# Performance work log

Measured on AMD Instinct MI355X. Metric: run time of the kernel, lower is better.

## Reference

```python
import jax, jax.numpy as jnp
import numpy as np
import math

MAX_REL_POS = 32  # max_relative_position

def _sincos_table(d_model, max_len):
    pos = np.arange(max_len)[:, None].astype(np.float32)
    div = np.exp(np.arange(0, d_model, 2).astype(np.float32) * (-math.log(10000.0) / d_model))
    pe = np.zeros((max_len, d_model), dtype=np.float32)
    pe[:, 0::2] = np.sin(pos * div)
    pe[:, 1::2] = np.cos(pos * div)
    return jnp.asarray(pe)

def setup_inputs() -> dict:
    rng = jax.random.key(0)
    k1, k2, k3 = jax.random.split(rng, 3)
    B, H, S, D = 4, 16, 1024, 64
    pe = _sincos_table(D, 2 * MAX_REL_POS + 1)  # fixed (non-trainable) buffer
    return {
        "query": jax.random.normal(k1, (B, H, S, D), jnp.float32),
        "key": jax.random.normal(k2, (B, H, S, D), jnp.float32),
        "value": jax.random.normal(k3, (B, H, S, D), jnp.float32),
        "pe_k": pe,
        "pe_v": pe,
    }

def reference(query, key, value, pe_k, pe_v):
    B, H, S, D = query.shape
    # relative distance indices: clip(k - q, -P, P) + P  -> [S, S]
    dist = jnp.clip(jnp.arange(S)[None, :] - jnp.arange(S)[:, None],
                    -MAX_REL_POS, MAX_REL_POS) + MAX_REL_POS
    R_k = pe_k[dist]  # [S, S, D]
    R_v = pe_v[dist]  # [S, S, D]
    scores = jnp.einsum('bhqd,bhkd->bhqk', query, key)
    scores = scores + jnp.einsum('bhqd,qkd->bhqk', query, R_k)
    scores = scores / math.sqrt(D)
    # one_direction=True -> causal mask
    causal = jnp.tril(jnp.ones((S, S), dtype=bool))
    scores = jnp.where(causal[None, None], scores, jnp.float32(-1e9))
    p_attn = jax.nn.softmax(scores, axis=-1)
    output = jnp.einsum('bhqk,bhkd->bhqd', p_attn, value)
    output = output + jnp.einsum('bhqv,qvd->bhqd', p_attn, R_v)
    return output, p_attn
```

## Files before the change

### kernel.cpp

```cpp
#include <hip/hip_runtime.h>

typedef __attribute__((ext_vector_type(8))) short bfrag;
typedef __attribute__((ext_vector_type(4))) float ffrag;

namespace {
constexpr int Sc = 1024, Dc = 64;
constexpr int P2 = 72;
constexpr int PQ = 64;
constexpr int PW = 33;
constexpr float SCALE = 0.125f;
}

__device__ __forceinline__ unsigned short f2bf(float f) {
    unsigned u = __builtin_bit_cast(unsigned, f);
    u += 0x7fffu + ((u >> 16) & 1u);
    return (unsigned short)(u >> 16);
}
__device__ __forceinline__ bfrag pack8(float4 a, float4 b) {
    bfrag r;
    r[0] = (short)f2bf(a.x); r[1] = (short)f2bf(a.y);
    r[2] = (short)f2bf(a.z); r[3] = (short)f2bf(a.w);
    r[4] = (short)f2bf(b.x); r[5] = (short)f2bf(b.y);
    r[6] = (short)f2bf(b.z); r[7] = (short)f2bf(b.w);
    return r;
}
#define MFMA(a, b, c) __builtin_amdgcn_mfma_f32_16x16x32_bf16((a), (b), (c), 0, 0, 0)

__global__ __launch_bounds__(256, 2)
void relattn(const float* __restrict__ Qg, const float* __restrict__ Kg,
             const float* __restrict__ Vg, const float* __restrict__ pek,
             const float* __restrict__ pev, float* __restrict__ outg,
             float* __restrict__ pbuf)
{
    __shared__ __align__(16) char smem[72448];
    unsigned short* Ks0 = (unsigned short*)smem;
    unsigned short* Ks1 = (unsigned short*)(smem + 9216);
    unsigned short* Vt0 = (unsigned short*)(smem + 18432);
    unsigned short* Vt1 = (unsigned short*)(smem + 27648);
    unsigned short* Pt0 = (unsigned short*)(smem + 36864);
    unsigned short* Pt1 = (unsigned short*)(smem + 46080);
    float* Ts = (float*)(smem + 55296);
    unsigned short* Qs = (unsigned short*)(smem + 63744);
    float* Ws = (float*)(smem + 63744);
    float* W0 = (float*)(smem + 72192);
    float* Ot = (float*)smem;

    const int tid  = threadIdx.x;
    const int bh   = blockIdx.y;
    const int wv   = tid >> 6;
    const int lane = tid & 63;
    const int n    = lane & 15;
    const int quad = lane >> 4;

    const float* Qbh = Qg + (size_t)bh * Sc * Dc;
    const float* Kbh = Kg + (size_t)bh * Sc * Dc;
    const float* Vbh = Vg + (size_t)bh * Sc * Dc;
    float* pbh = pbuf + (size_t)bh * Sc * Sc;
    float* obh = outg + (size_t)bh * Sc * Dc;

    const int sr  = tid >> 2;
    const int sc4 = (tid & 3) * 16;
    const int kp  = tid & 31;
    const int vd0 = (tid >> 5) * 8;

    const int rr = tid >> 4;
    const int c4 = tid & 15;

    for (int half = 0; half < 2; ++half) {
        const int qt = half ? (15 - (int)blockIdx.x) : (int)blockIdx.x;
        const int qrow = wv * 16 + quad * 4;

        __syncthreads();

        float4 k0a, k0b, k0c, k0d;
        {
            const float* ksrc = Kbh + (size_t)sr * Dc + sc4;
            k0a = *(const float4*)(ksrc);
            k0b = *(const float4*)(ksrc + 4);
            k0c = *(const float4*)(ksrc + 8);
            k0d = *(const float4*)(ksrc + 12);
        }
        {
            const float* src = Qbh + (size_t)(qt * 64 + sr) * Dc + sc4;
            float4 a = *(const float4*)(src);
            float4 b = *(const float4*)(src + 4);
            float4 c = *(const float4*)(src + 8);
            float4 d = *(const float4*)(src + 12);
            *(bfrag*)&Qs[sr * PQ + sc4]     = pack8(a, b);
            *(bfrag*)&Qs[sr * PQ + sc4 + 8] = pack8(c, d);
        }
        for (int i = tid; i < 135; i += 256) {
            bfrag z = {};
            *(bfrag*)&Ks0[33 * P2 + i * 8] = z;
        }
        if (tid < 132) {
            int r = tid >> 2, c0 = (tid & 3) * 16;
            const float* src = pek + (size_t)r * Dc + c0;
            float4 a = *(const float4*)(src);
            float4 b = *(const float4*)(src + 4);
            float4 c = *(const float4*)(src + 8);
            float4 d = *(const float4*)(src + 12);
            *(bfrag*)&Ks0[r * P2 + c0]     = pack8(a, b);
            *(bfrag*)&Ks0[r * P2 + c0 + 8] = pack8(c, d);
        }
        __syncthreads();

        bfrag qa0 = *(bfrag*)&Qs[(wv * 16 + n) * PQ + quad * 8];
        bfrag qa1 = *(bfrag*)&Qs[(wv * 16 + n) * PQ + 32 + quad * 8];

        #pragma unroll
        for (int sub = 0; sub < 3; ++sub) {
            bfrag b0 = *(bfrag*)&Ks0[(sub * 16 + n) * P2 + quad * 8];
            bfrag b1 = *(bfrag*)&Ks0[(sub * 16 + n) * P2 + 32 + quad * 8];
            ffrag c = {};
            c = MFMA(qa0, b0, c);
            c = MFMA(qa1, b1, c);
            int j = sub * 16 + n;
            if (j <= 32) {
                #pragma unroll
                for (int reg = 0; reg < 4; ++reg)
                    Ts[(qrow + reg) * PW + j] = c[reg];
            }
        }
        *(bfrag*)&Ks1[sr * P2 + sc4]     = pack8(k0a, k0b);
        *(bfrag*)&Ks1[sr * P2 + sc4 + 8] = pack8(k0c, k0d);
        float4 pka, pkb, pkc, pkd;
        if (qt >= 1) {
            const float* ksrc = Kbh + (size_t)(64 + sr) * Dc + sc4;
            pka = *(const float4*)(ksrc);
            pkb = *(const float4*)(ksrc + 4);
            pkc = *(const float4*)(ksrc + 8);
            pkd = *(const float4*)(ksrc + 12);
        }
        __syncthreads();

        float ts0[4];
        #pragma unroll
        for (int reg = 0; reg < 4; ++reg) ts0[reg] = Ts[(qrow + reg) * PW];

        for (int idx = tid; idx < 64 * PW; idx += 256) Ws[idx] = 0.f;

        {
            const int zb = (qt + 1) * 64;
            if (zb < Sc) {
                const int z4 = (Sc - zb) >> 2;
                const float4 z = make_float4(0.f, 0.f, 0.f, 0.f);
                for (int r = 0; r < 64; ++r) {
                    float4* rp = (float4*)(pbh + (size_t)(qt * 64 + r) * Sc + zb);
                    for (int cz = tid; cz < z4; cz += 256) rp[cz] = z;
                }
            }
        }

        float lsum[4] = {0.f, 0.f, 0.f, 0.f};
        for (int kt = 0; kt <= qt; ++kt) {
            const bool bnd = (kt >= qt - 1);
            unsigned short* Kc = (kt & 1) ? Ks0 : Ks1;
            unsigned short* Kn = (kt & 1) ? Ks1 : Ks0;
            #pragma unroll
            for (int sub = 0; sub < 4; ++sub) {
                bfrag b0 = *(bfrag*)&Kc[(sub * 16 + n) * P2 + quad * 8];
                bfrag b1 = *(bfrag*)&Kc[(sub * 16 + n) * P2 + 32 + quad * 8];
                ffrag c = {};
                c = MFMA(qa0, b0, c);
                c = MFMA(qa1, b1, c);
                const int k = kt * 64 + sub * 16 + n;
                if (!bnd) {
                    #pragma unroll
                    for (int reg = 0; reg < 4; ++reg)
                        lsum[reg] += __expf((c[reg] + ts0[reg]) * SCALE);
                } else {
                    #pragma unroll
                    for (int reg = 0; reg < 4; ++reg) {
                        int jrel = k - (qt * 64 + qrow + reg) + 32;
                        if (jrel <= 32) {
                            int jcl = jrel < 0 ? 0 : jrel;
                            lsum[reg] += __expf((c[reg] + Ts[(qrow + reg) * PW + jcl]) * SCALE);
                        }
                    }
                }
            }
            if (kt < qt) {
                *(bfrag*)&Kn[sr * P2 + sc4]     = pack8(pka, pkb);
                *(bfrag*)&Kn[sr * P2 + sc4 + 8] = pack8(pkc, pkd);
            }
            if (kt + 2 <= qt) {
                const float* ksrc = Kbh + (size_t)((kt + 2) * 64 + sr) * Dc + sc4;
                pka = *(const float4*)(ksrc);
                pkb = *(const float4*)(ksrc + 4);
                pkc = *(const float4*)(ksrc + 8);
                pkd = *(const float4*)(ksrc + 12);
            }
            __syncthreads();
        }
        float rinv[4];
        #pragma unroll
        for (int reg = 0; reg < 4; ++reg) {
            float l = lsum[reg];
            l += __shfl_xor(l, 1);
            l += __shfl_xor(l, 2);
            l += __shfl_xor(l, 4);
            l += __shfl_xor(l, 8);
            rinv[reg] = 1.f / l;
        }

        {
            const float* ksrc = Kbh + (size_t)sr * Dc + sc4;
            float4 a = *(const float4*)(ksrc);
            float4 b = *(const float4*)(ksrc + 4);
            float4 c = *(const float4*)(ksrc + 8);
            float4 d = *(const float4*)(ksrc + 12);
            *(bfrag*)&Ks0[sr * P2 + sc4]     = pack8(a, b);
            *(bfrag*)&Ks0[sr * P2 + sc4 + 8] = pack8(c, d);
        }
        if (qt >= 1) {
            const float* ksrc = Kbh + (size_t)(64 + sr) * Dc + sc4;
            pka = *(const float4*)(ksrc);
            pkb = *(const float4*)(ksrc + 4);
            pkc = *(const float4*)(ksrc + 8);
            pkd = *(const float4*)(ksrc + 12);
        }
        float4 pva, pvb, pvc, pvd;
        {
            const float* vsrc = Vbh + (size_t)(2 * kp) * Dc + vd0;
            pva = *(const float4*)(vsrc);
            pvb = *(const float4*)(vsrc + 4);
            pvc = *(const float4*)(vsrc + Dc);
            pvd = *(const float4*)(vsrc + Dc + 4);
        }
        __syncthreads();

        ffrag oacc[4];
        #pragma unroll
        for (int i = 0; i < 4; ++i) { ffrag z = {}; oacc[i] = z; }

        for (int kt = 0; kt <= qt; ++kt) {
            const bool bnd = (kt >= qt - 1);
            unsigned short* Kc  = (kt & 1) ? Ks1 : Ks0;
            unsigned short* Kn  = (kt & 1) ? Ks0 : Ks1;
            unsigned short* Vc  = (kt & 1) ? Vt1 : Vt0;
            unsigned short* Vp  = (kt & 1) ? Vt0 : Vt1;
            unsigned short* Ptc = (kt & 1) ? Pt1 : Pt0;
            unsigned short* Ptp = (kt & 1) ? Pt0 : Pt1;

            #pragma unroll
            for (int sub = 0; sub < 4; ++sub) {
                bfrag b0 = *(bfrag*)&Kc[(sub * 16 + n) * P2 + quad * 8];
                bfrag b1 = *(bfrag*)&Kc[(sub * 16 + n) * P2 + 32 + quad * 8];
                ffrag c = {};
                c = MFMA(qa0, b0, c);
                c = MFMA(qa1, b1, c);
                const int k = kt * 64 + sub * 16 + n;
                if (!bnd) {
                    #pragma unroll
                    for (int reg = 0; reg < 4; ++reg) {
                        float p = __expf((c[reg] + ts0[reg]) * SCALE) * rinv[reg];
                        Ptc[(qrow + reg) * P2 + sub * 16 + n] = (unsigned short)f2bf(p);
                    }
                } else {
                    #pragma unroll
                    for (int reg = 0; reg < 4; ++reg) {
                        int jrel = k - (qt * 64 + qrow + reg) + 32;
                        float p = 0.f;
                        if (jrel <= 32) {
                            int jcl = jrel < 0 ? 0 : jrel;
                            p = __expf((c[reg] + Ts[(qrow + reg) * PW + jcl]) * SCALE) * rinv[reg];
                        }
                        Ptc[(qrow + reg) * P2 + sub * 16 + n] = (unsigned short)f2bf(p);
                        if ((unsigned)(jrel - 1) < 32u) Ws[(qrow + reg) * PW + jrel - 1] = p;
                    }
                }
            }
            if (kt < qt) {
                *(bfrag*)&Kn[sr * P2 + sc4]     = pack8(pka, pkb);
                *(bfrag*)&Kn[sr * P2 + sc4 + 8] = pack8(pkc, pkd);
            }
            {
                float r0[8] = {pva.x, pva.y, pva.z, pva.w, pvb.x, pvb.y, pvb.z, pvb.w};
                float r1[8] = {pvc.x, pvc.y, pvc.z, pvc.w, pvd.x, pvd.y, pvd.z, pvd.w};
                #pragma unroll
                for (int i = 0; i < 8; ++i) {
                    unsigned pk = (unsigned)f2bf(r0[i]) | ((unsigned)f2bf(r1[i]) << 16);
                    *(unsigned*)&Vc[(vd0 + i) * P2 + 2 * kp] = pk;
                }
            }
            if (kt + 2 <= qt) {
                const float* ksrc = Kbh + (size_t)((kt + 2) * 64 + sr) * Dc + sc4;
                pka = *(const float4*)(ksrc);
                pkb = *(const float4*)(ksrc + 4);
                pkc = *(const float4*)(ksrc + 8);
                pkd = *(const float4*)(ksrc + 12);
            }
            if (kt + 1 <= qt) {
                const float* vsrc = Vbh + (size_t)((kt + 1) * 64 + 2 * kp) * Dc + vd0;
                pva = *(const float4*)(vsrc);
                pvb = *(const float4*)(vsrc + 4);
                pvc = *(const float4*)(vsrc + Dc);
                pvd = *(const float4*)(vsrc + Dc + 4);
            }
            if (kt >= 1) {
                bfrag pb0 = *(bfrag*)&Ptp[(wv * 16 + n) * P2 + quad * 8];
                bfrag pb1 = *(bfrag*)&Ptp[(wv * 16 + n) * P2 + 32 + quad * 8];
                #pragma unroll
                for (int ds = 0; ds < 4; ++ds) {
                    bfrag va0 = *(bfrag*)&Vp[(ds * 16 + n) * P2 + quad * 8];
                    bfrag va1 = *(bfrag*)&Vp[(ds * 16 + n) * P2 + 32 + quad * 8];
                    oacc[ds] = MFMA(va0, pb0, oacc[ds]);
                    oacc[ds] = MFMA(va1, pb1, oacc[ds]);
                }
                float* base = pbh + ((size_t)(qt * 64 + rr) * Sc + (kt - 1) * 64 + c4 * 4);
                #pragma unroll
                for (int step = 0; step < 4; ++step) {
                    const int r = step * 16 + rr;
                    const unsigned short* ps = &Ptp[r * P2 + c4 * 4];
                    unsigned two0 = *(const unsigned*)(ps);
                    unsigned two1 = *(const unsigned*)(ps + 2);
                    float4 v;
                    v.x = __builtin_bit_cast(float, (two0 & 0xffffu) << 16);
                    v.y = __builtin_bit_cast(float, two0 & 0xffff0000u);
                    v.z = __builtin_bit_cast(float, (two1 & 0xffffu) << 16);
                    v.w = __builtin_bit_cast(float, two1 & 0xffff0000u);
                    *(float4*)(base + (size_t)(step * 16) * Sc) = v;
                }
            }
            __syncthreads();
        }
        {
            unsigned short* Ptp = (qt & 1) ? Pt1 : Pt0;
            unsigned short* Vp  = (qt & 1) ? Vt1 : Vt0;
            bfrag pb0 = *(bfrag*)&Ptp[(wv * 16 + n) * P2 + quad * 8];
            bfrag pb1 = *(bfrag*)&Ptp[(wv * 16 + n) * P2 + 32 + quad * 8];
            #pragma unroll
            for (int ds = 0; ds < 4; ++ds) {
                bfrag va0 = *(bfrag*)&Vp[(ds * 16 + n) * P2 + quad * 8];
                bfrag va1 = *(bfrag*)&Vp[(ds * 16 + n) * P2 + 32 + quad * 8];
                oacc[ds] = MFMA(va0, pb0, oacc[ds]);
                oacc[ds] = MFMA(va1, pb1, oacc[ds]);
            }
            float* base = pbh + ((size_t)(qt * 64 + rr) * Sc + qt * 64 + c4 * 4);
            #pragma unroll
            for (int step = 0; step < 4; ++step) {
                const int r = step * 16 + rr;
                const unsigned short* ps = &Ptp[r * P2 + c4 * 4];
                unsigned two0 = *(const unsigned*)(ps);
                unsigned two1 = *(const unsigned*)(ps + 2);
                float4 v;
                v.x = __builtin_bit_cast(float, (two0 & 0xffffu) << 16);
                v.y = __builtin_bit_cast(float, two0 & 0xffff0000u);
                v.z = __builtin_bit_cast(float, (two1 & 0xffffu) << 16);
                v.w = __builtin_bit_cast(float, two1 & 0xffff0000u);
                *(float4*)(base + (size_t)(step * 16) * Sc) = v;
            }
        }
        __syncthreads();

        if (tid < 64) {
            float s = 0.f;
            #pragma unroll
            for (int j = 0; j < 32; ++j) s += Ws[tid * PW + j];
            W0[tid] = 1.f - s;
        }
        {
            int q = tid >> 2, j0 = (tid & 3) * 8;
            #pragma unroll
            for (int i = 0; i < 8; i += 2) {
                unsigned pk = (unsigned)f2bf(Ws[q * PW + j0 + i]) |
                              ((unsigned)f2bf(Ws[q * PW + j0 + i + 1]) << 16);
                *(unsigned*)&Pt0[q * P2 + j0 + i] = pk;
            }
        }
        {
            int jj = tid >> 3, d0 = (tid & 7) * 8;
            const float* src = pev + (size_t)(jj + 1) * Dc + d0;
            float4 a = *(const float4*)(src);
            float4 b = *(const float4*)(src + 4);
            float vr[8] = {a.x, a.y, a.z, a.w, b.x, b.y, b.z, b.w};
            #pragma unroll
            for (int i = 0; i < 8; ++i)
                Vt0[(d0 + i) * P2 + jj] = (unsigned short)f2bf(vr[i]);
        }
        __syncthreads();
        {
            bfrag pb = *(bfrag*)&Pt0[(wv * 16 + n) * P2 + quad * 8];
            #pragma unroll
            for (int ds = 0; ds < 4; ++ds) {
                bfrag va = *(bfrag*)&Vt0[(ds * 16 + n) * P2 + quad * 8];
                oacc[ds] = MFMA(va, pb, oacc[ds]);
            }
        }
        float w0q = W0[wv * 16 + n];
        #pragma unroll
        for (int ds = 0; ds < 4; ++ds) {
            float4 ov;
            ov.x = oacc[ds][0] + w0q * pev[ds * 16 + quad * 4 + 0];
            ov.y = oacc[ds][1] + w0q * pev[ds * 16 + quad * 4 + 1];
            ov.z = oacc[ds][2] + w0q * pev[ds * 16 + quad * 4 + 2];
            ov.w = oacc[ds][3] + w0q * pev[ds * 16 + quad * 4 + 3];
            *(float4*)&Ot[(wv * 16 + n) * 68 + ds * 16 + quad * 4] = ov;
        }
        __syncthreads();
        {
            int r = tid >> 2, c0 = (tid & 3) * 16;
            float* dst = obh + (size_t)(qt * 64 + r) * Dc + c0;
            *(float4*)(dst)      = *(float4*)&Ot[r * 68 + c0];
            *(float4*)(dst + 4)  = *(float4*)&Ot[r * 68 + c0 + 4];
            *(float4*)(dst + 8)  = *(float4*)&Ot[r * 68 + c0 + 8];
            *(float4*)(dst + 12) = *(float4*)&Ot[r * 68 + c0 + 12];
        }
    }
}

extern "C" void kernel_launch(void* const* d_in, const int* in_sizes, int n_in,
                              void* d_out, int out_size, void* d_ws, size_t ws_size,
                              hipStream_t stream)
{
    const float* Q   = (const float*)d_in[0];
    const float* K   = (const float*)d_in[1];
    const float* V   = (const float*)d_in[2];
    const float* pek = (const float*)d_in[3];
    const float* pev = (const float*)d_in[4];
    float* out  = (float*)d_out;
    float* pbuf = out + (size_t)64 * Sc * Dc;

    dim3 grid(8, 64);
    relattn<<<grid, 256, 0, stream>>>(Q, K, V, pek, pev, out, pbuf);
}
```

Measured before the change: 373.8 us.

## Double block size to 512 threads, splitting key and value columns across wave pairs

The block grows from 4 to 8 waves. Each pair of waves shares a 16-row query strip and splits the key columns (scores) and value columns (output) between them. Softmax row sums become partial per wave and are combined through a small new shared-memory buffer before normalization. Tile loads and stores are spread over twice as many threads, each moving half as much data. The goal is more waves in flight per CU to hide global-memory latency, especially for the large probability-matrix writes. In exchange it adds a shared-memory reduction and a tighter register budget from the new launch bounds.

```diff
diff --git a/kernel.cpp b/kernel.cpp
--- a/kernel.cpp
+++ b/kernel.cpp
@@ -26,13 +26,13 @@
 }
 #define MFMA(a, b, c) __builtin_amdgcn_mfma_f32_16x16x32_bf16((a), (b), (c), 0, 0, 0)
 
-__global__ __launch_bounds__(256, 2)
+__global__ __launch_bounds__(512, 4)
 void relattn(const float* __restrict__ Qg, const float* __restrict__ Kg,
              const float* __restrict__ Vg, const float* __restrict__ pek,
              const float* __restrict__ pev, float* __restrict__ outg,
              float* __restrict__ pbuf)
 {
-    __shared__ __align__(16) char smem[72448];
+    __shared__ __align__(16) char smem[72960];
     unsigned short* Ks0 = (unsigned short*)smem;
     unsigned short* Ks1 = (unsigned short*)(smem + 9216);
     unsigned short* Vt0 = (unsigned short*)(smem + 18432);
@@ -43,6 +43,7 @@
     unsigned short* Qs = (unsigned short*)(smem + 63744);
     float* Ws = (float*)(smem + 63744);
     float* W0 = (float*)(smem + 72192);
+    float* Lp = (float*)(smem + 72448);
     float* Ot = (float*)smem;
 
     const int tid  = threadIdx.x;
@@ -51,6 +52,8 @@
     const int lane = tid & 63;
     const int n    = lane & 15;
     const int quad = lane >> 4;
+    const int wr   = wv >> 1;
+    const int wc   = wv & 1;
 
     const float* Qbh = Qg + (size_t)bh * Sc * Dc;
     const float* Kbh = Kg + (size_t)bh * Sc * Dc;
@@ -58,79 +61,71 @@
     float* pbh = pbuf + (size_t)bh * Sc * Sc;
     float* obh = outg + (size_t)bh * Sc * Dc;
 
-    const int sr  = tid >> 2;
-    const int sc4 = (tid & 3) * 16;
+    const int sr  = tid >> 3;
+    const int sc8 = (tid & 7) * 8;
     const int kp  = tid & 31;
-    const int vd0 = (tid >> 5) * 8;
+    const int vd0 = (tid >> 5) * 4;
 
     const int rr = tid >> 4;
     const int c4 = tid & 15;
 
     for (int half = 0; half < 2; ++half) {
         const int qt = half ? (15 - (int)blockIdx.x) : (int)blockIdx.x;
-        const int qrow = wv * 16 + quad * 4;
-
-        __syncthreads();
-
-        float4 k0a, k0b, k0c, k0d;
-        {
-            const float* ksrc = Kbh + (size_t)sr * Dc + sc4;
+        const int qrow = wr * 16 + quad * 4;
+
+        __syncthreads();
+
+        float4 k0a, k0b;
+        {
+            const float* ksrc = Kbh + (size_t)sr * Dc + sc8;
             k0a = *(const float4*)(ksrc);
             k0b = *(const float4*)(ksrc + 4);
-            k0c = *(const float4*)(ksrc + 8);
-            k0d = *(const float4*)(ksrc + 12);
-        }
-        {
-            const float* src = Qbh + (size_t)(qt * 64 + sr) * Dc + sc4;
+        }
+        {
+            const float* src = Qbh + (size_t)(qt * 64 + sr) * Dc + sc8;
             float4 a = *(const float4*)(src);
             float4 b = *(const float4*)(src + 4);
-            float4 c = *(const float4*)(src + 8);
-            float4 d = *(const float4*)(src + 12);
-            *(bfrag*)&Qs[sr * PQ + sc4]     = pack8(a, b);
-            *(bfrag*)&Qs[sr * PQ + sc4 + 8] = pack8(c, d);
-        }
-        for (int i = tid; i < 135; i += 256) {
+            *(bfrag*)&Qs[sr * PQ + sc8] = pack8(a, b);
+        }
+        if (tid < 135) {
             bfrag z = {};
-            *(bfrag*)&Ks0[33 * P2 + i * 8] = z;
-        }
-        if (tid < 132) {
-            int r = tid >> 2, c0 = (tid & 3) * 16;
+            *(bfrag*)&Ks0[33 * P2 + tid * 8] = z;
+        }
+        if (tid < 264) {
+            int r = tid >> 3, c0 = (tid & 7) * 8;
             const float* src = pek + (size_t)r * Dc + c0;
             float4 a = *(const float4*)(src);
             float4 b = *(const float4*)(src + 4);
-            float4 c = *(const float4*)(src + 8);
-            float4 d = *(const float4*)(src + 12);
-            *(bfrag*)&Ks0[r * P2 + c0]     = pack8(a, b);
-            *(bfrag*)&Ks0[r * P2 + c0 + 8] = pack8(c, d);
-        }
-        __syncthreads();
-
-        bfrag qa0 = *(bfrag*)&Qs[(wv * 16 + n) * PQ + quad * 8];
-        bfrag qa1 = *(bfrag*)&Qs[(wv * 16 + n) * PQ + 32 + quad * 8];
-
-        #pragma unroll
-        for (int sub = 0; sub < 3; ++sub) {
-            bfrag b0 = *(bfrag*)&Ks0[(sub * 16 + n) * P2 + quad * 8];
-            bfrag b1 = *(bfrag*)&Ks0[(sub * 16 + n) * P2 + 32 + quad * 8];
-            ffrag c = {};
-            c = MFMA(qa0, b0, c);
-            c = MFMA(qa1, b1, c);
-            int j = sub * 16 + n;
-            if (j <= 32) {
-                #pragma unroll
-                for (int reg = 0; reg < 4; ++reg)
-                    Ts[(qrow + reg) * PW + j] = c[reg];
-            }
-        }
-        *(bfrag*)&Ks1[sr * P2 + sc4]     = pack8(k0a, k0b);
-        *(bfrag*)&Ks1[sr * P2 + sc4 + 8] = pack8(k0c, k0d);
-        float4 pka, pkb, pkc, pkd;
+            *(bfrag*)&Ks0[r * P2 + c0] = pack8(a, b);
+        }
+        __syncthreads();
+
+        bfrag qa0 = *(bfrag*)&Qs[(wr * 16 + n) * PQ + quad * 8];
+        bfrag qa1 = *(bfrag*)&Qs[(wr * 16 + n) * PQ + 32 + quad * 8];
+
+        #pragma unroll
+        for (int si = 0; si < 2; ++si) {
+            const int sub = wc * 2 + si;
+            if (sub < 3) {
+                bfrag b0 = *(bfrag*)&Ks0[(sub * 16 + n) * P2 + quad * 8];
+                bfrag b1 = *(bfrag*)&Ks0[(sub * 16 + n) * P2 + 32 + quad * 8];
+                ffrag c = {};
+                c = MFMA(qa0, b0, c);
+                c = MFMA(qa1, b1, c);
+                int j = sub * 16 + n;
+                if (j <= 32) {
+                    #pragma unroll
+                    for (int reg = 0; reg < 4; ++reg)
+                        Ts[(qrow + reg) * PW + j] = c[reg];
+                }
+            }
+        }
+        *(bfrag*)&Ks1[sr * P2 + sc8] = pack8(k0a, k0b);
+        float4 pka, pkb;
         if (qt >= 1) {
-            const float* ksrc = Kbh + (size_t)(64 + sr) * Dc + sc4;
+            const float* ksrc = Kbh + (size_t)(64 + sr) * Dc + sc8;
             pka = *(const float4*)(ksrc);
             pkb = *(const float4*)(ksrc + 4);
-            pkc = *(const float4*)(ksrc + 8);
-            pkd = *(const float4*)(ksrc + 12);
         }
         __syncthreads();
 
@@ -138,7 +133,7 @@
         #pragma unroll
         for (int reg = 0; reg < 4; ++reg) ts0[reg] = Ts[(qrow + reg) * PW];
 
-        for (int idx = tid; idx < 64 * PW; idx += 256) Ws[idx] = 0.f;
+        for (int idx = tid; idx < 64 * PW; idx += 512) Ws[idx] = 0.f;
 
         {
             const int zb = (qt + 1) * 64;
@@ -147,7 +142,7 @@
                 const float4 z = make_float4(0.f, 0.f, 0.f, 0.f);
                 for (int r = 0; r < 64; ++r) {
                     float4* rp = (float4*)(pbh + (size_t)(qt * 64 + r) * Sc + zb);
-                    for (int cz = tid; cz < z4; cz += 256) rp[cz] = z;
+                    for (int cz = tid; cz < z4; cz += 512) rp[cz] = z;
                 }
             }
         }
@@ -158,7 +153,8 @@
             unsigned short* Kc = (kt & 1) ? Ks0 : Ks1;
             unsigned short* Kn = (kt & 1) ? Ks1 : Ks0;
             #pragma unroll
-            for (int sub = 0; sub < 4; ++sub) {
+            for (int si = 0; si < 2; ++si) {
+                const int sub = wc * 2 + si;
                 bfrag b0 = *(bfrag*)&Kc[(sub * 16 + n) * P2 + quad * 8];
                 bfrag b1 = *(bfrag*)&Kc[(sub * 16 + n) * P2 + 32 + quad * 8];
                 ffrag c = {};
@@ -180,20 +176,15 @@
                     }
                 }
             }
-            if (kt < qt) {
-                *(bfrag*)&Kn[sr * P2 + sc4]     = pack8(pka, pkb);
-                *(bfrag*)&Kn[sr * P2 + sc4 + 8] = pack8(pkc, pkd);
-            }
+            if (kt < qt)
+                *(bfrag*)&Kn[sr * P2 + sc8] = pack8(pka, pkb);
             if (kt + 2 <= qt) {
-                const float* ksrc = Kbh + (size_t)((kt + 2) * 64 + sr) * Dc + sc4;
+                const float* ksrc = Kbh + (size_t)((kt + 2) * 64 + sr) * Dc + sc8;
                 pka = *(const float4*)(ksrc);
                 pkb = *(const float4*)(ksrc + 4);
-                pkc = *(const float4*)(ksrc + 8);
-                pkd = *(const float4*)(ksrc + 12);
             }
             __syncthreads();
         }
-        float rinv[4];
         #pragma unroll
         for (int reg = 0; reg < 4; ++reg) {
             float l = lsum[reg];
@@ -201,38 +192,41 @@
             l += __shfl_xor(l, 2);
             l += __shfl_xor(l, 4);
             l += __shfl_xor(l, 8);
-            rinv[reg] = 1.f / l;
-        }
-
-        {
-            const float* ksrc = Kbh + (size_t)sr * Dc + sc4;
+            lsum[reg] = l;
+        }
+        if (n == 0) {
+            #pragma unroll
+            for (int reg = 0; reg < 4; ++reg)
+                Lp[wc * 64 + qrow + reg] = lsum[reg];
+        }
+
+        {
+            const float* ksrc = Kbh + (size_t)sr * Dc + sc8;
             float4 a = *(const float4*)(ksrc);
             float4 b = *(const float4*)(ksrc + 4);
-            float4 c = *(const float4*)(ksrc + 8);
-            float4 d = *(const float4*)(ksrc + 12);
-            *(bfrag*)&Ks0[sr * P2 + sc4]     = pack8(a, b);
-            *(bfrag*)&Ks0[sr * P2 + sc4 + 8] = pack8(c, d);
+            *(bfrag*)&Ks0[sr * P2 + sc8] = pack8(a, b);
         }
         if (qt >= 1) {
-            const float* ksrc = Kbh + (size_t)(64 + sr) * Dc + sc4;
+            const float* ksrc = Kbh + (size_t)(64 + sr) * Dc + sc8;
             pka = *(const float4*)(ksrc);
             pkb = *(const float4*)(ksrc + 4);
-            pkc = *(const float4*)(ksrc + 8);
-            pkd = *(const float4*)(ksrc + 12);
-        }
-        float4 pva, pvb, pvc, pvd;
+        }
+        float4 pva, pvb;
         {
             const float* vsrc = Vbh + (size_t)(2 * kp) * Dc + vd0;
             pva = *(const float4*)(vsrc);
-            pvb = *(const float4*)(vsrc + 4);
-            pvc = *(const float4*)(vsrc + Dc);
-            pvd = *(const float4*)(vsrc + Dc + 4);
-        }
-        __syncthreads();
-
-        ffrag oacc[4];
-        #pragma unroll
-        for (int i = 0; i < 4; ++i) { ffrag z = {}; oacc[i] = z; }
+            pvb = *(const float4*)(vsrc + Dc);
+        }
+        __syncthreads();
+
+        float rinv[4];
+        #pragma unroll
+        for (int reg = 0; reg < 4; ++reg)
+            rinv[reg] = 1.f / (Lp[qrow + reg] + Lp[64 + qrow + reg]);
+
+        ffrag oacc[2];
+        #pragma unroll
+        for (int i = 0; i < 2; ++i) { ffrag z = {}; oacc[i] = z; }
 
         for (int kt = 0; kt <= qt; ++kt) {
             const bool bnd = (kt >= qt - 1);
@@ -244,7 +238,8 @@
             unsigned short* Ptp = (kt & 1) ? Pt0 : Pt1;
 
             #pragma unroll
-            for (int sub = 0; sub < 4; ++sub) {
+            for (int si = 0; si < 2; ++si) {
+                const int sub = wc * 2 + si;
                 bfrag b0 = *(bfrag*)&Kc[(sub * 16 + n) * P2 + quad * 8];
                 bfrag b1 = *(bfrag*)&Kc[(sub * 16 + n) * P2 + 32 + quad * 8];
                 ffrag c = {};
@@ -271,47 +266,42 @@
                     }
                 }
             }
-            if (kt < qt) {
-                *(bfrag*)&Kn[sr * P2 + sc4]     = pack8(pka, pkb);
-                *(bfrag*)&Kn[sr * P2 + sc4 + 8] = pack8(pkc, pkd);
-            }
+            if (kt < qt)
+                *(bfrag*)&Kn[sr * P2 + sc8] = pack8(pka, pkb);
             {
-                float r0[8] = {pva.x, pva.y, pva.z, pva.w, pvb.x, pvb.y, pvb.z, pvb.w};
-                float r1[8] = {pvc.x, pvc.y, pvc.z, pvc.w, pvd.x, pvd.y, pvd.z, pvd.w};
+                float r0[4] = {pva.x, pva.y, pva.z, pva.w};
+                float r1[4] = {pvb.x, pvb.y, pvb.z, pvb.w};
                 #pragma unroll
-                for (int i = 0; i < 8; ++i) {
+                for (int i = 0; i < 4; ++i) {
                     unsigned pk = (unsigned)f2bf(r0[i]) | ((unsigned)f2bf(r1[i]) << 16);
                     *(unsigned*)&Vc[(vd0 + i) * P2 + 2 * kp] = pk;
                 }
             }
             if (kt + 2 <= qt) {
-                const float* ksrc = Kbh + (size_t)((kt + 2) * 64 + sr) * Dc + sc4;
+                const float* ksrc = Kbh + (size_t)((kt + 2) * 64 + sr) * Dc + sc8;
                 pka = *(const float4*)(ksrc);
                 pkb = *(const float4*)(ksrc + 4);
-                pkc = *(const float4*)(ksrc + 8);
-                pkd = *(const float4*)(ksrc + 12);
             }
             if (kt + 1 <= qt) {
                 const float* vsrc = Vbh + (size_t)((kt + 1) * 64 + 2 * kp) * Dc + vd0;
                 pva = *(const float4*)(vsrc);
-                pvb = *(const float4*)(vsrc + 4);
-                pvc = *(const float4*)(vsrc + Dc);
-                pvd = *(const float4*)(vsrc + Dc + 4);
+                pvb = *(const float4*)(vsrc + Dc);
             }
             if (kt >= 1) {
-                bfrag pb0 = *(bfrag*)&Ptp[(wv * 16 + n) * P2 + quad * 8];
-                bfrag pb1 = *(bfrag*)&Ptp[(wv * 16 + n) * P2 + 32 + quad * 8];
+                bfrag pb0 = *(bfrag*)&Ptp[(wr * 16 + n) * P2 + quad * 8];
+                bfrag pb1 = *(bfrag*)&Ptp[(wr * 16 + n) * P2 + 32 + quad * 8];
                 #pragma unroll
-                for (int ds = 0; ds < 4; ++ds) {
+                for (int dsi = 0; dsi < 2; ++dsi) {
+                    const int ds = wc * 2 + dsi;
                     bfrag va0 = *(bfrag*)&Vp[(ds * 16 + n) * P2 + quad * 8];
                     bfrag va1 = *(bfrag*)&Vp[(ds * 16 + n) * P2 + 32 + quad * 8];
-                    oacc[ds] = MFMA(va0, pb0, oacc[ds]);
-                    oacc[ds] = MFMA(va1, pb1, oacc[ds]);
+                    oacc[dsi] = MFMA(va0, pb0, oacc[dsi]);
+                    oacc[dsi] = MFMA(va1, pb1, oacc[dsi]);
                 }
                 float* base = pbh + ((size_t)(qt * 64 + rr) * Sc + (kt - 1) * 64 + c4 * 4);
                 #pragma unroll
-                for (int step = 0; step < 4; ++step) {
-                    const int r = step * 16 + rr;
+                for (int step = 0; step < 2; ++step) {
+                    const int r = step * 32 + rr;
                     const unsigned short* ps = &Ptp[r * P2 + c4 * 4];
                     unsigned two0 = *(const unsigned*)(ps);
                     unsigned two1 = *(const unsigned*)(ps + 2);
@@ -320,7 +310,7 @@
                     v.y = __builtin_bit_cast(float, two0 & 0xffff0000u);
                     v.z = __builtin_bit_cast(float, (two1 & 0xffffu) << 16);
                     v.w = __builtin_bit_cast(float, two1 & 0xffff0000u);
-                    *(float4*)(base + (size_t)(step * 16) * Sc) = v;
+                    *(float4*)(base + (size_t)(step * 32) * Sc) = v;
                 }
             }
             __syncthreads();
@@ -328,19 +318,20 @@
         {
             unsigned short* Ptp = (qt & 1) ? Pt1 : Pt0;
             unsigned short* Vp  = (qt & 1) ? Vt1 : Vt0;
-            bfrag pb0 = *(bfrag*)&Ptp[(wv * 16 + n) * P2 + quad * 8];
-            bfrag pb1 = *(bfrag*)&Ptp[(wv * 16 + n) * P2 + 32 + quad * 8];
-            #pragma unroll
-            for (int ds = 0; ds < 4; ++ds) {
+            bfrag pb0 = *(bfrag*)&Ptp[(wr * 16 + n) * P2 + quad * 8];
+            bfrag pb1 = *(bfrag*)&Ptp[(wr * 16 + n) * P2 + 32 + quad * 8];
+            #pragma unroll
+            for (int dsi = 0; dsi < 2; ++dsi) {
+                const int ds = wc * 2 + dsi;
                 bfrag va0 = *(bfrag*)&Vp[(ds * 16 + n) * P2 + quad * 8];
                 bfrag va1 = *(bfrag*)&Vp[(ds * 16 + n) * P2 + 32 + quad * 8];
-                oacc[ds] = MFMA(va0, pb0, oacc[ds]);
-                oacc[ds] = MFMA(va1, pb1, oacc[ds]);
+                oacc[dsi] = MFMA(va0, pb0, oacc[dsi]);
+                oacc[dsi] = MFMA(va1, pb1, oacc[dsi]);
             }
             float* base = pbh + ((size_t)(qt * 64 + rr) * Sc + qt * 64 + c4 * 4);
             #pragma unroll
-            for (int step = 0; step < 4; ++step) {
-                const int r = step * 16 + rr;
+            for (int step = 0; step < 2; ++step) {
+                const int r = step * 32 + rr;
                 const unsigned short* ps = &Ptp[r * P2 + c4 * 4];
                 unsigned two0 = *(const unsigned*)(ps);
                 unsigned two1 = *(const unsigned*)(ps + 2);
@@ -349,7 +340,7 @@
                 v.y = __builtin_bit_cast(float, two0 & 0xffff0000u);
                 v.z = __builtin_bit_cast(float, (two1 & 0xffffu) << 16);
                 v.w = __builtin_bit_cast(float, two1 & 0xffff0000u);
-                *(float4*)(base + (size_t)(step * 16) * Sc) = v;
+                *(float4*)(base + (size_t)(step * 32) * Sc) = v;
             }
         }
         __syncthreads();
@@ -361,51 +352,50 @@
             W0[tid] = 1.f - s;
         }
         {
-            int q = tid >> 2, j0 = (tid & 3) * 8;
-            #pragma unroll
-            for (int i = 0; i < 8; i += 2) {
-                unsigned pk = (unsigned)f2bf(Ws[q * PW + j0 + i]) |
-                              ((unsigned)f2bf(Ws[q * PW + j0 + i + 1]) << 16);
-                *(unsigned*)&Pt0[q * P2 + j0 + i] = pk;
-            }
-        }
-        {
-            int jj = tid >> 3, d0 = (tid & 7) * 8;
+            int q = tid >> 3, j0 = (tid & 7) * 4;
+            unsigned pk0 = (unsigned)f2bf(Ws[q * PW + j0]) |
+                           ((unsigned)f2bf(Ws[q * PW + j0 + 1]) << 16);
+            unsigned pk1 = (unsigned)f2bf(Ws[q * PW + j0 + 2]) |
+                           ((unsigned)f2bf(Ws[q * PW + j0 + 3]) << 16);
+            *(unsigned*)&Pt0[q * P2 + j0]     = pk0;
+            *(unsigned*)&Pt0[q * P2 + j0 + 2] = pk1;
+        }
+        {
+            int jj = tid >> 4, d0 = (tid & 15) * 4;
             const float* src = pev + (size_t)(jj + 1) * Dc + d0;
             float4 a = *(const float4*)(src);
-            float4 b = *(const float4*)(src + 4);
-            float vr[8] = {a.x, a.y, a.z, a.w, b.x, b.y, b.z, b.w};
-            #pragma unroll
-            for (int i = 0; i < 8; ++i)
+            float vr[4] = {a.x, a.y, a.z, a.w};
+            #pragma unroll
+            for (int i = 0; i < 4; ++i)
                 Vt0[(d0 + i) * P2 + jj] = (unsigned short)f2bf(vr[i]);
         }
         __syncthreads();
         {
-            bfrag pb = *(bfrag*)&Pt0[(wv * 16 + n) * P2 + quad * 8];
-            #pragma unroll
-            for (int ds = 0; ds < 4; ++ds) {
+            bfrag pb = *(bfrag*)&Pt0[(wr * 16 + n) * P2 + quad * 8];
+            #pragma unroll
+            for (int dsi = 0; dsi < 2; ++dsi) {
+                const int ds = wc * 2 + dsi;
                 bfrag va = *(bfrag*)&Vt0[(ds * 16 + n) * P2 + quad * 8];
-                oacc[ds] = MFMA(va, pb, oacc[ds]);
-            }
-        }
-        float w0q = W0[wv * 16 + n];
-        #pragma unroll
-        for (int ds = 0; ds < 4; ++ds) {
+                oacc[dsi] = MFMA(va, pb, oacc[dsi]);
+            }
+        }
+        float w0q = W0[wr * 16 + n];
+        #pragma unroll
+        for (int dsi = 0; dsi < 2; ++dsi) {
+            const int ds = wc * 2 + dsi;
             float4 ov;
-            ov.x = oacc[ds][0] + w0q * pev[ds * 16 + quad * 4 + 0];
-            ov.y = oacc[ds][1] + w0q * pev[ds * 16 + quad * 4 + 1];
-            ov.z = oacc[ds][2] + w0q * pev[ds * 16 + quad * 4 + 2];
-            ov.w = oacc[ds][3] + w0q * pev[ds * 16 + quad * 4 + 3];
-            *(float4*)&Ot[(wv * 16 + n) * 68 + ds * 16 + quad * 4] = ov;
-        }
-        __syncthreads();
-        {
-            int r = tid >> 2, c0 = (tid & 3) * 16;
+            ov.x = oacc[dsi][0] + w0q * pev[ds * 16 + quad * 4 + 0];
+            ov.y = oacc[dsi][1] + w0q * pev[ds * 16 + quad * 4 + 1];
+            ov.z = oacc[dsi][2] + w0q * pev[ds * 16 + quad * 4 + 2];
+            ov.w = oacc[dsi][3] + w0q * pev[ds * 16 + quad * 4 + 3];
+            *(float4*)&Ot[(wr * 16 + n) * 68 + ds * 16 + quad * 4] = ov;
+        }
+        __syncthreads();
+        {
+            int r = tid >> 3, c0 = (tid & 7) * 8;
             float* dst = obh + (size_t)(qt * 64 + r) * Dc + c0;
-            *(float4*)(dst)      = *(float4*)&Ot[r * 68 + c0];
-            *(float4*)(dst + 4)  = *(float4*)&Ot[r * 68 + c0 + 4];
-            *(float4*)(dst + 8)  = *(float4*)&Ot[r * 68 + c0 + 8];
-            *(float4*)(dst + 12) = *(float4*)&Ot[r * 68 + c0 + 12];
+            *(float4*)(dst)     = *(float4*)&Ot[r * 68 + c0];
+            *(float4*)(dst + 4) = *(float4*)&Ot[r * 68 + c0 + 4];
         }
     }
 }
@@ -423,5 +413,5 @@
     float* pbuf = out + (size_t)64 * Sc * Dc;
 
     dim3 grid(8, 64);
-    relattn<<<grid, 256, 0, stream>>>(Q, K, V, pek, pev, out, pbuf);
+    relattn<<<grid, 512, 0, stream>>>(Q, K, V, pek, pev, out, pbuf);
 }
```

Measured after the change: 395.3 us. 1.06x slower.
